# Kernel tuning notes

Hardware: AMD Instinct MI355X
Metric: run time of the kernel (lower is better)

The kernel has to match this reference:

```python
import jax, jax.numpy as jnp
import numpy as np

N, E, B, D, Q, C = 50000, 250000, 128, 302, 600, 2000
NEG_SLOPE = 0.2  # PyG GATConv default


def setup_inputs() -> dict:
    key = jax.random.key(0)
    ks = jax.random.split(key, 12)
    x = jax.random.normal(ks[0], (N, D), jnp.float32)
    edges = jax.random.randint(ks[1], (2, E), 0, N, dtype=jnp.int32)
    query = jax.random.normal(ks[2], (B, Q), jnp.float32)
    batch = jnp.sort(jax.random.randint(ks[3], (N,), 0, B, dtype=jnp.int32))
    # GATConv(302, 302, heads=1) params (shared across the 3 applications)
    theta = jax.random.normal(ks[4], (D, D), jnp.float32) / np.float32(np.sqrt(D))
    att_src = jax.random.normal(ks[5], (D,), jnp.float32) * 0.1
    att_dst = jax.random.normal(ks[6], (D,), jnp.float32) * 0.1
    gat_bias = jnp.zeros((D,), jnp.float32)
    # Attention.W ~ torch.rand(decoder_dim, encoder_dim) -> stored as [Q, D]
    attW = jax.random.uniform(ks[7], (Q, D), jnp.float32)
    lin_w = jax.random.normal(ks[8], (C, D), jnp.float32) / np.float32(np.sqrt(D))
    lin_b = jnp.zeros((C,), jnp.float32)
    return {"x": x, "edges": edges, "query": query, "batch": batch,
            "theta": theta, "att_src": att_src, "att_dst": att_dst,
            "gat_bias": gat_bias, "attW": attW, "lin_w": lin_w, "lin_b": lin_b}


def _segment_softmax(s, seg, num_segments):
    m = jax.ops.segment_max(s, seg, num_segments=num_segments)
    ex = jnp.exp(s - m[seg])
    den = jax.ops.segment_sum(ex, seg, num_segments=num_segments)
    return ex / den[seg]


def reference(x, edges, query, batch, theta, att_src, att_dst, gat_bias, attW, lin_w, lin_b):
    # add self loops once (PyG GATConv add_self_loops=True)
    loops = jnp.arange(N, dtype=edges.dtype)
    src = jnp.concatenate([edges[0], loops])
    dst = jnp.concatenate([edges[1], loops])

    def gat(h_in):
        h = h_in @ theta.T                       # [N, D]
        a_s = h @ att_src                        # [N]
        a_d = h @ att_dst                        # [N]
        e = jax.nn.leaky_relu(a_s[src] + a_d[dst], NEG_SLOPE)  # [E+N]
        alpha = _segment_softmax(e, dst, N)      # softmax over incoming edges
        out = jax.ops.segment_sum(alpha[:, None] * h[src], dst, num_segments=N)
        return out + gat_bias

    h = jax.nn.relu(gat(x))
    h = jax.nn.relu(gat(h))
    h = jax.nn.relu(gat(h))                      # [N, D]

    # Attention pooling: score_j = (query[batch_j] @ W) . h_j / sqrt(Q)
    qp = query @ attW                            # [B, D]
    s = jnp.sum(qp[batch] * h, axis=-1) / np.float32(np.sqrt(Q))  # [N]
    w = _segment_softmax(s, batch, B)            # per-graph softmax weights
    pooled = jax.ops.segment_sum(w[:, None] * h, batch, num_segments=B)  # [B, D]

    return jax.nn.relu(pooled) @ lin_w.T + lin_b  # [B, C]
```

## Files before the change

kernel.cpp:

```cpp
#include <hip/hip_runtime.h>
#include <hip/hip_bf16.h>
#include <math.h>

#define N_NODES 50000
#define N_EDGES 250000
#define BB      128
#define DD      302
#define QQ      600
#define CC      2000
#define NEG_SLOPE 0.2f
#define GS      304
#define KP      320
#define KSTEPS  10
#define PC      64
#define BPK_KS  20480

typedef __attribute__((ext_vector_type(8))) short short8;
typedef __attribute__((ext_vector_type(4))) float f32x4;

__device__ __forceinline__ void gload_lds16(const void* g, void* l) {
    __builtin_amdgcn_global_load_lds((const __attribute__((address_space(1))) void*)g,
                                     (__attribute__((address_space(3))) void*)l, 16, 0, 0);
}

__device__ __host__ __forceinline__ int bswz(int q, int n) {
    return q ^ (n & 3) ^ ((n >> 2) & 3);
}

__global__ void k_deg_init(int* deg, int* cursor) {
    int i = blockIdx.x * blockDim.x + threadIdx.x;
    if (i < N_NODES) { deg[i] = 1; cursor[i] = 0; }
}

__global__ void k_histogram(const int* __restrict__ dst, int* deg) {
    int e = blockIdx.x * blockDim.x + threadIdx.x;
    if (e < N_EDGES) atomicAdd(&deg[dst[e]], 1);
}

__global__ void k_scan_block(const int* __restrict__ deg, int* offs, int* partials) {
    __shared__ int sh[256];
    int i = blockIdx.x * 256 + threadIdx.x;
    int v = (i < N_NODES) ? deg[i] : 0;
    sh[threadIdx.x] = v;
    __syncthreads();
    for (int d = 1; d < 256; d <<= 1) {
        int t = (threadIdx.x >= d) ? sh[threadIdx.x - d] : 0;
        __syncthreads();
        sh[threadIdx.x] += t;
        __syncthreads();
    }
    if (i < N_NODES) offs[i] = sh[threadIdx.x] - v;
    if (threadIdx.x == 255) partials[blockIdx.x] = sh[255];
}

__global__ void k_scan_partials(int* partials, int nb) {
    __shared__ int sh[256];
    int v = (threadIdx.x < nb) ? partials[threadIdx.x] : 0;
    sh[threadIdx.x] = v;
    __syncthreads();
    for (int d = 1; d < 256; d <<= 1) {
        int t = (threadIdx.x >= d) ? sh[threadIdx.x - d] : 0;
        __syncthreads();
        sh[threadIdx.x] += t;
        __syncthreads();
    }
    if (threadIdx.x < nb) partials[threadIdx.x] = sh[threadIdx.x] - v;
}

__global__ void k_scan_add(int* offs, const int* __restrict__ partials) {
    int i = blockIdx.x * 256 + threadIdx.x;
    if (i < N_NODES) offs[i] += partials[blockIdx.x];
}

__global__ void k_scatter(const int* __restrict__ src, const int* __restrict__ dst,
                          const int* __restrict__ offs, int* cursor, int* esrc) {
    int i = blockIdx.x * blockDim.x + threadIdx.x;
    if (i < N_EDGES) {
        int d = dst[i];
        int pos = offs[d] + atomicAdd(&cursor[d], 1);
        esrc[pos] = src[i];
    } else if (i < N_EDGES + N_NODES) {
        int n = i - N_EDGES;
        int pos = offs[n] + atomicAdd(&cursor[n], 1);
        esrc[pos] = n;
    }
}

__global__ void k_theta_prep(const float* __restrict__ theta,
                             const float* __restrict__ att_src,
                             const float* __restrict__ att_dst,
                             unsigned short* __restrict__ bpk) {
    if (blockIdx.x >= 400) {
        int k = (blockIdx.x - 400) * 256 + threadIdx.x;
        if (k >= KP) return;
        float vs = 0.f, vd = 0.f;
        if (k < DD) {
            for (int j = 0; j < DD; j++) {
                float t = theta[j * DD + k];
                vs += t * att_src[j];
                vd += t * att_dst[j];
            }
        }
        int ks = k >> 5, kk = k & 31, q = kk >> 3, kb = kk & 7;
        size_t b0 = (size_t)ks * BPK_KS + DD * 32 + bswz(q, DD) * 8 + kb;
        size_t b1 = (size_t)ks * BPK_KS + (DD + 1) * 32 + bswz(q, DD + 1) * 8 + kb;
        unsigned int u, uh, ul;
        u  = __float_as_uint(vs);
        uh = (u + 0x8000u) & 0xffff0000u;
        ul = (__float_as_uint(vs - __uint_as_float(uh)) + 0x8000u) >> 16;
        bpk[b0]         = (unsigned short)(uh >> 16);
        bpk[b0 + 10240] = (unsigned short)ul;
        u  = __float_as_uint(vd);
        uh = (u + 0x8000u) & 0xffff0000u;
        ul = (__float_as_uint(vd - __uint_as_float(uh)) + 0x8000u) >> 16;
        bpk[b1]         = (unsigned short)(uh >> 16);
        bpk[b1 + 10240] = (unsigned short)ul;
        return;
    }
    int idx = blockIdx.x * 256 + threadIdx.x;
    if (idx >= KP * KP) return;
    int n = idx / KP, k = idx % KP;
    if (n == DD || n == DD + 1) return;
    float v = (n < DD && k < DD) ? theta[n * DD + k] : 0.f;
    unsigned int u  = __float_as_uint(v);
    unsigned int uh = (u + 0x8000u) & 0xffff0000u;
    float hf = __uint_as_float(uh);
    float lo = v - hf;
    unsigned int ul = (__float_as_uint(lo) + 0x8000u) >> 16;
    int ks = k >> 5, kk = k & 31, q = kk >> 3, kb = kk & 7;
    size_t base = (size_t)ks * BPK_KS + n * 32 + bswz(q, n) * 8 + kb;
    bpk[base]         = (unsigned short)(uh >> 16);
    bpk[base + 10240] = (unsigned short)ul;
}

__global__ __launch_bounds__(256) void k_mfma_gemm(const float* __restrict__ A, int lda,
                                                   const unsigned short* __restrict__ Bpk,
                                                   float* __restrict__ C,
                                                   float* __restrict__ a_s,
                                                   float* __restrict__ a_d, int M) {
    __shared__ __attribute__((aligned(16))) unsigned short Bs[2][BPK_KS];

    const int tid   = threadIdx.x;
    const int lane  = tid & 63;
    const int wave  = tid >> 6;
    const int q     = lane >> 4;
    const int mr    = lane & 15;
    const int m0    = blockIdx.x * 64;
    const int nbase = wave * 80;
    const int kvalid = (lda == GS) ? GS : DD;

    f32x4 acc[4][5];
    #pragma unroll
    for (int i = 0; i < 4; i++)
        #pragma unroll
        for (int j = 0; j < 5; j++)
            acc[i][j] = (f32x4){0.f, 0.f, 0.f, 0.f};

    const float* arow[4];
    bool rok[4];
    #pragma unroll
    for (int mt = 0; mt < 4; mt++) {
        int row = m0 + mt * 16 + mr;
        rok[mt]  = row < M;
        arow[mt] = A + (size_t)(row < M ? row : 0) * lda;
    }

    const char* gB = (const char*)Bpk;

    auto loadA = [&](float (&f)[4][8], int ks) {
        const int k0c = ks * 32 + q * 8;
        #pragma unroll
        for (int mt = 0; mt < 4; mt++) {
            if (rok[mt] && (k0c + 8 <= kvalid)) {
                float4 v0 = *(const float4*)(arow[mt] + k0c);
                float4 v1 = *(const float4*)(arow[mt] + k0c + 4);
                f[mt][0]=v0.x; f[mt][1]=v0.y; f[mt][2]=v0.z; f[mt][3]=v0.w;
                f[mt][4]=v1.x; f[mt][5]=v1.y; f[mt][6]=v1.z; f[mt][7]=v1.w;
            } else {
                #pragma unroll
                for (int p = 0; p < 8; p += 2) {
                    int k = k0c + p;
                    float2 t = {0.f, 0.f};
                    if (rok[mt] && k < kvalid) t = *(const float2*)(arow[mt] + k);
                    f[mt][p] = t.x; f[mt][p+1] = t.y;
                }
            }
        }
    };

    auto stageB = [&](int buf, int ks) {
        const char* gsrc = gB + (size_t)(ks * BPK_KS) * 2;
        #pragma unroll
        for (int j = 0; j < 10; j++) {
            int chunk = j * 4 + wave;
            gload_lds16(gsrc + chunk * 1024 + lane * 16,
                        (char*)Bs[buf] + chunk * 1024);
        }
    };

    float fcur[4][8], fnext[4][8];

    loadA(fcur, 0);
    stageB(0, 0);
    __syncthreads();

    #pragma unroll
    for (int ks = 0; ks < KSTEPS; ks++) {
        if (ks + 1 < KSTEPS) {
            stageB((ks + 1) & 1, ks + 1);
            loadA(fnext, ks + 1);
        }

        short8 ah[4], al[4];
        #pragma unroll
        for (int mt = 0; mt < 4; mt++) {
            #pragma unroll
            for (int p = 0; p < 8; p++) {
                unsigned int u  = __float_as_uint(fcur[mt][p]);
                unsigned int uh = (u + 0x8000u) & 0xffff0000u;
                float l = fcur[mt][p] - __uint_as_float(uh);
                ah[mt][p] = (short)(uh >> 16);
                al[mt][p] = (short)((__float_as_uint(l) + 0x8000u) >> 16);
            }
        }

        const unsigned short* Bc = Bs[ks & 1];
        short8 bh[5], bl[5];
        #pragma unroll
        for (int nt = 0; nt < 5; nt++) {
            int col = nbase + nt * 16 + mr;
            int off = col * 32 + bswz(q, col) * 8;
            bh[nt] = *(const short8*)&Bc[off];
            bl[nt] = *(const short8*)&Bc[10240 + off];
        }
        #pragma unroll
        for (int nt = 0; nt < 5; nt++) {
            #pragma unroll
            for (int mt = 0; mt < 4; mt++) {
                acc[mt][nt] = __builtin_amdgcn_mfma_f32_16x16x32_bf16(ah[mt], bh[nt], acc[mt][nt], 0, 0, 0);
                acc[mt][nt] = __builtin_amdgcn_mfma_f32_16x16x32_bf16(ah[mt], bl[nt], acc[mt][nt], 0, 0, 0);
                acc[mt][nt] = __builtin_amdgcn_mfma_f32_16x16x32_bf16(al[mt], bh[nt], acc[mt][nt], 0, 0, 0);
            }
        }

        __syncthreads();

        #pragma unroll
        for (int mt = 0; mt < 4; mt++)
            #pragma unroll
            for (int p = 0; p < 8; p++)
                fcur[mt][p] = fnext[mt][p];
    }

    #pragma unroll
    for (int mt = 0; mt < 4; mt++) {
        int row_b = m0 + mt * 16 + q * 4;
        #pragma unroll
        for (int nt = 0; nt < 5; nt++) {
            int col = nbase + nt * 16 + mr;
            if (col > DD + 1) continue;
            #pragma unroll
            for (int r = 0; r < 4; r++) {
                int row = row_b + r;
                if (row >= M) continue;
                float v = acc[mt][nt][r];
                if (col < DD) {
                    C[(size_t)row * GS + col] = v;
                } else if (col == DD) {
                    a_s[row] = v;
                    C[(size_t)row * GS + DD] = 0.f;
                } else {
                    a_d[row] = v;
                    C[(size_t)row * GS + DD + 1] = 0.f;
                }
            }
        }
    }
}

#define BM 64
#define BN 64
#define BK 16
__global__ __launch_bounds__(256) void k_gemm_nt(const float* __restrict__ A,
                                                 const float* __restrict__ B,
                                                 float* __restrict__ C,
                                                 int M, int N, int K,
                                                 const float* __restrict__ bias,
                                                 int relu_a) {
    __shared__ float As[BK][BM + 4];
    __shared__ float Bs[BK][BN + 4];
    int m0 = blockIdx.y * BM;
    int n0 = blockIdx.x * BN;
    int tid = threadIdx.x;
    int tr = tid >> 4;
    int tc = tid & 15;
    float acc[4][4] = {};
    for (int k0 = 0; k0 < K; k0 += BK) {
        #pragma unroll
        for (int j = 0; j < 4; j++) {
            int e = tid + 256 * j;
            int r = e >> 4;
            int k = e & 15;
            int gk = k0 + k;
            int gm = m0 + r;
            float va = 0.f;
            if (gm < M && gk < K) va = A[(size_t)gm * K + gk];
            if (relu_a) va = fmaxf(va, 0.f);
            As[k][r] = va;
            int gn = n0 + r;
            float vb = 0.f;
            if (gn < N && gk < K) vb = B[(size_t)gn * K + gk];
            Bs[k][r] = vb;
        }
        __syncthreads();
        #pragma unroll
        for (int k = 0; k < BK; k++) {
            float a[4], b[4];
            #pragma unroll
            for (int i = 0; i < 4; i++) a[i] = As[k][tr * 4 + i];
            #pragma unroll
            for (int j = 0; j < 4; j++) b[j] = Bs[k][tc * 4 + j];
            #pragma unroll
            for (int i = 0; i < 4; i++)
                #pragma unroll
                for (int j = 0; j < 4; j++)
                    acc[i][j] += a[i] * b[j];
        }
        __syncthreads();
    }
    #pragma unroll
    for (int i = 0; i < 4; i++) {
        int gm = m0 + tr * 4 + i;
        if (gm >= M) continue;
        #pragma unroll
        for (int j = 0; j < 4; j++) {
            int gn = n0 + tc * 4 + j;
            if (gn < N) {
                float v = acc[i][j];
                if (bias) v += bias[gn];
                C[(size_t)gm * N + gn] = v;
            }
        }
    }
}

__global__ __launch_bounds__(256) void k_qp(const float* __restrict__ query,
                                            const float* __restrict__ attW,
                                            float* __restrict__ qp) {
    int b = blockIdx.y;
    int d = blockIdx.x * 256 + threadIdx.x;
    if (d >= DD) return;
    const float* qrow = query + (size_t)b * QQ;
    float acc = 0.f;
    #pragma unroll 8
    for (int q = 0; q < QQ; q++) acc += qrow[q] * attW[(size_t)q * DD + d];
    qp[(size_t)b * DD + d] = acc;
}

__global__ __launch_bounds__(256) void k_aggregate(const float* __restrict__ h,
                                                   const float* __restrict__ a_s,
                                                   const float* __restrict__ a_d,
                                                   const int* __restrict__ offs,
                                                   const int* __restrict__ deg,
                                                   const int* __restrict__ esrc,
                                                   const float* __restrict__ bias,
                                                   float* __restrict__ out,
                                                   const float* __restrict__ qp,
                                                   const int* __restrict__ batch,
                                                   float* __restrict__ sarr) {
    int gid = blockIdx.x * blockDim.x + threadIdx.x;
    int n = gid >> 6, lane = gid & 63;
    if (n >= N_NODES) return;
    int beg = offs[n], cnt = deg[n];
    float adn = a_d[n];
    float m = -INFINITY;
    for (int i = lane; i < cnt; i += 64) {
        float e = a_s[esrc[beg + i]] + adn;
        e = (e > 0.f) ? e : NEG_SLOPE * e;
        m = fmaxf(m, e);
    }
    for (int off = 32; off; off >>= 1) m = fmaxf(m, __shfl_xor(m, off));
    float den = 0.f;
    for (int i = lane; i < cnt; i += 64) {
        float e = a_s[esrc[beg + i]] + adn;
        e = (e > 0.f) ? e : NEG_SLOPE * e;
        den += __expf(e - m);
    }
    for (int off = 32; off; off >>= 1) den += __shfl_xor(den, off);
    float inv_den = 1.f / den;

    const int c0 = lane * 4;
    const int c1 = 256 + lane * 4;
    const bool has1 = lane < 12;
    float4 A0 = {0.f, 0.f, 0.f, 0.f};
    float4 A1 = {0.f, 0.f, 0.f, 0.f};
    for (int i = 0; i < cnt; i++) {
        int s = esrc[beg + i];
        float e = a_s[s] + adn;
        e = (e > 0.f) ? e : NEG_SLOPE * e;
        float w = __expf(e - m) * inv_den;
        const float* row = h + (size_t)s * GS;
        float4 r0 = *(const float4*)(row + c0);
        A0.x += w * r0.x; A0.y += w * r0.y; A0.z += w * r0.z; A0.w += w * r0.w;
        if (has1) {
            float4 r1 = *(const float4*)(row + c1);
            A1.x += w * r1.x; A1.y += w * r1.y; A1.z += w * r1.z; A1.w += w * r1.w;
        }
    }
    float4 o0, o1 = {0.f, 0.f, 0.f, 0.f};
    {
        float4 b0 = *(const float4*)(bias + c0);
        o0.x = fmaxf(A0.x + b0.x, 0.f);
        o0.y = fmaxf(A0.y + b0.y, 0.f);
        o0.z = fmaxf(A0.z + b0.z, 0.f);
        o0.w = fmaxf(A0.w + b0.w, 0.f);
        *(float4*)(out + (size_t)n * GS + c0) = o0;
    }
    if (lane < 11) {
        float4 b1 = *(const float4*)(bias + c1);
        o1.x = fmaxf(A1.x + b1.x, 0.f);
        o1.y = fmaxf(A1.y + b1.y, 0.f);
        o1.z = fmaxf(A1.z + b1.z, 0.f);
        o1.w = fmaxf(A1.w + b1.w, 0.f);
        *(float4*)(out + (size_t)n * GS + c1) = o1;
    } else if (lane == 11) {
        o1.x = fmaxf(A1.x + bias[300], 0.f);
        o1.y = fmaxf(A1.y + bias[301], 0.f);
        o1.z = 0.f;
        o1.w = 0.f;
        *(float4*)(out + (size_t)n * GS + 300) = o1;
    }

    if (sarr) {
        const float* qv = qp + (size_t)batch[n] * DD;
        float d = o0.x * qv[c0] + o0.y * qv[c0 + 1] + o0.z * qv[c0 + 2] + o0.w * qv[c0 + 3];
        if (lane < 11)
            d += o1.x * qv[c1] + o1.y * qv[c1 + 1] + o1.z * qv[c1 + 2] + o1.w * qv[c1 + 3];
        else if (lane == 11)
            d += o1.x * qv[300] + o1.y * qv[301];
        for (int off = 32; off; off >>= 1) d += __shfl_xor(d, off);
        if (lane == 0) sarr[n] = d * 0.04082482904638630f;
    }
}

__global__ void k_gbounds(const int* __restrict__ batch, int* goffs, int* gcnt) {
    __shared__ int bound[BB + 1];
    int b = threadIdx.x;
    if (b <= BB) {
        int lo = 0, hi = N_NODES;
        while (lo < hi) {
            int mid = (lo + hi) >> 1;
            if (batch[mid] < b) lo = mid + 1; else hi = mid;
        }
        bound[b] = lo;
    }
    __syncthreads();
    if (b < BB) {
        goffs[b] = bound[b];
        gcnt[b]  = bound[b + 1] - bound[b];
    }
}

__global__ __launch_bounds__(256) void k_gstats(const float* __restrict__ sarr,
                                                const int* __restrict__ goffs,
                                                const int* __restrict__ gcnt,
                                                float* __restrict__ wn,
                                                float* __restrict__ pooled) {
    int b = blockIdx.x;
    int beg = goffs[b], cnt = gcnt[b];
    __shared__ float red[256];
    float m = -INFINITY;
    for (int i = threadIdx.x; i < cnt; i += 256) m = fmaxf(m, sarr[beg + i]);
    red[threadIdx.x] = m;
    __syncthreads();
    for (int d = 128; d; d >>= 1) {
        if (threadIdx.x < d) red[threadIdx.x] = fmaxf(red[threadIdx.x], red[threadIdx.x + d]);
        __syncthreads();
    }
    m = red[0];
    __syncthreads();
    float den = 0.f;
    for (int i = threadIdx.x; i < cnt; i += 256) den += __expf(sarr[beg + i] - m);
    red[threadIdx.x] = den;
    __syncthreads();
    for (int d = 128; d; d >>= 1) {
        if (threadIdx.x < d) red[threadIdx.x] += red[threadIdx.x + d];
        __syncthreads();
    }
    float dinv = (cnt > 0) ? 1.f / red[0] : 0.f;
    for (int i = threadIdx.x; i < cnt; i += 256)
        wn[beg + i] = __expf(sarr[beg + i] - m) * dinv;
    for (int j = threadIdx.x; j < DD; j += 256)
        pooled[(size_t)b * DD + j] = 0.f;
}

__global__ __launch_bounds__(256) void k_poolacc(const float* __restrict__ h, int ld,
                                                 const float* __restrict__ wn,
                                                 const int* __restrict__ batch,
                                                 float* __restrict__ pooled) {
    int c0 = blockIdx.x * PC;
    if (c0 >= N_NODES) return;
    int nmax = N_NODES - c0; if (nmax > PC) nmax = PC;
    __shared__ int   sb[PC];
    __shared__ float sw[PC];
    for (int i = threadIdx.x; i < nmax; i += 256) {
        sb[i] = batch[c0 + i];
        sw[i] = wn[c0 + i];
    }
    __syncthreads();
    int f0 = threadIdx.x, f1 = threadIdx.x + 256;
    float a0 = 0.f, a1 = 0.f;
    int g = sb[0];
    for (int i = 0; i < nmax; i++) {
        int bi = sb[i];
        if (bi != g) {
            if (f0 < DD) atomicAdd(&pooled[(size_t)g * DD + f0], a0);
            if (f1 < DD) atomicAdd(&pooled[(size_t)g * DD + f1], a1);
            a0 = 0.f; a1 = 0.f; g = bi;
        }
        float w = sw[i];
        const float* row = h + (size_t)(c0 + i) * ld;
        if (f0 < DD) a0 += w * row[f0];
        if (f1 < DD) a1 += w * row[f1];
    }
    if (f0 < DD) atomicAdd(&pooled[(size_t)g * DD + f0], a0);
    if (f1 < DD) atomicAdd(&pooled[(size_t)g * DD + f1], a1);
}

extern "C" void kernel_launch(void* const* d_in, const int* in_sizes, int n_in,
                              void* d_out, int out_size, void* d_ws, size_t ws_size,
                              hipStream_t stream) {
    const float* x        = (const float*)d_in[0];
    const int*   edges    = (const int*)d_in[1];
    const float* query    = (const float*)d_in[2];
    const int*   batch    = (const int*)d_in[3];
    const float* theta    = (const float*)d_in[4];
    const float* att_src  = (const float*)d_in[5];
    const float* att_dst  = (const float*)d_in[6];
    const float* gat_bias = (const float*)d_in[7];
    const float* attW     = (const float*)d_in[8];
    const float* lin_w    = (const float*)d_in[9];
    const float* lin_b    = (const float*)d_in[10];
    float* out = (float*)d_out;

    char* ws = (char*)d_ws;
    size_t off = 0;
    auto alloc = [&](size_t bytes) -> void* {
        off = (off + 255) & ~(size_t)255;
        void* p = ws + off;
        off += bytes;
        return p;
    };

    float* G    = (float*)alloc((size_t)N_NODES * GS * 4);
    float* P    = (float*)alloc((size_t)N_NODES * GS * 4);
    unsigned short* bpk = (unsigned short*)alloc((size_t)KSTEPS * BPK_KS * 2);
    float* a_s  = (float*)alloc((size_t)N_NODES * 4);
    float* a_d  = (float*)alloc((size_t)N_NODES * 4);
    float* sarr = (float*)alloc((size_t)N_NODES * 4);
    float* wn   = (float*)alloc((size_t)N_NODES * 4);
    int* deg    = (int*)alloc((size_t)N_NODES * 4);
    int* cursor = (int*)alloc((size_t)N_NODES * 4);
    int* offs   = (int*)alloc((size_t)N_NODES * 4);
    int* esrc   = (int*)alloc((size_t)(N_EDGES + N_NODES) * 4);
    int* partials = (int*)alloc(256 * 4);
    int* gcnt   = (int*)alloc(BB * 4);
    int* goffs  = (int*)alloc(BB * 4);
    float* qp   = (float*)alloc((size_t)BB * DD * 4);
    float* pooled = (float*)alloc((size_t)BB * DD * 4);

    const int* e_src = edges;
    const int* e_dst = edges + N_EDGES;

    const int NB_SCAN = (N_NODES + 255) / 256;

    k_deg_init<<<NB_SCAN, 256, 0, stream>>>(deg, cursor);
    k_histogram<<<(N_EDGES + 255) / 256, 256, 0, stream>>>(e_dst, deg);
    k_scan_block<<<NB_SCAN, 256, 0, stream>>>(deg, offs, partials);
    k_scan_partials<<<1, 256, 0, stream>>>(partials, NB_SCAN);
    k_scan_add<<<NB_SCAN, 256, 0, stream>>>(offs, partials);
    k_scatter<<<(N_EDGES + N_NODES + 255) / 256, 256, 0, stream>>>(e_src, e_dst, offs, cursor, esrc);

    k_theta_prep<<<402, 256, 0, stream>>>(theta, att_src, att_dst, bpk);

    {
        dim3 g((DD + 255) / 256, BB);
        k_qp<<<g, 256, 0, stream>>>(query, attW, qp);
    }

    int mfma_blocks = (N_NODES + 63) / 64;
    int wave_blocks = (N_NODES + 3) / 4;
    const float* cur = x;
    int cur_ld = DD;
    for (int layer = 0; layer < 3; layer++) {
        k_mfma_gemm<<<mfma_blocks, 256, 0, stream>>>(cur, cur_ld, bpk, G, a_s, a_d, N_NODES);
        bool last = (layer == 2);
        k_aggregate<<<wave_blocks, 256, 0, stream>>>(G, a_s, a_d, offs, deg, esrc, gat_bias, P,
                                                     last ? qp : (const float*)nullptr,
                                                     last ? batch : (const int*)nullptr,
                                                     last ? sarr : (float*)nullptr);
        cur = P;
        cur_ld = GS;
    }

    k_gbounds<<<1, 256, 0, stream>>>(batch, goffs, gcnt);
    k_gstats<<<BB, 256, 0, stream>>>(sarr, goffs, gcnt, wn, pooled);
    k_poolacc<<<(N_NODES + PC - 1) / PC, 256, 0, stream>>>(P, GS, wn, batch, pooled);
    {
        dim3 g((CC + BN - 1) / BN, (BB + BM - 1) / BM);
        k_gemm_nt<<<g, 256, 0, stream>>>(pooled, lin_w, out, BB, CC, DD, lin_b, 1);
    }
}
```

Baseline: 732.3 us.

## Cut launches in CSR build and pooling; use online softmax in aggregation

Drops the scan-add pass by folding block partials and the self-loop offset into the CSR index math, and writes self-loops directly after each node's edges. The qp GEMV is merged into the theta-prep launch, the graph-bounds kernel is folded into gstats, and the degree/cursor init kernel becomes memsets. In the aggregation kernel, the separate max and sum passes over incoming edges become a single online-softmax pass, and the main edge loop gets a small unroll. The aim is less launch overhead and one less gather pass over esrc and a_s. The cost is slightly more index arithmetic and redundant binary searches per block. An unused leftover k_theta_prep variant with dummy code is left behind.

```diff
diff --git a/kernel.cpp b/kernel.cpp
--- a/kernel.cpp
+++ b/kernel.cpp
@@ -27,11 +27,6 @@
     return q ^ (n & 3) ^ ((n >> 2) & 3);
 }
 
-__global__ void k_deg_init(int* deg, int* cursor) {
-    int i = blockIdx.x * blockDim.x + threadIdx.x;
-    if (i < N_NODES) { deg[i] = 1; cursor[i] = 0; }
-}
-
 __global__ void k_histogram(const int* __restrict__ dst, int* deg) {
     int e = blockIdx.x * blockDim.x + threadIdx.x;
     if (e < N_EDGES) atomicAdd(&deg[dst[e]], 1);
@@ -67,29 +62,101 @@
     if (threadIdx.x < nb) partials[threadIdx.x] = sh[threadIdx.x] - v;
 }
 
-__global__ void k_scan_add(int* offs, const int* __restrict__ partials) {
-    int i = blockIdx.x * 256 + threadIdx.x;
-    if (i < N_NODES) offs[i] += partials[blockIdx.x];
-}
-
 __global__ void k_scatter(const int* __restrict__ src, const int* __restrict__ dst,
-                          const int* __restrict__ offs, int* cursor, int* esrc) {
+                          const int* __restrict__ offs, const int* __restrict__ partials,
+                          const int* __restrict__ deg, int* cursor, int* esrc) {
     int i = blockIdx.x * blockDim.x + threadIdx.x;
     if (i < N_EDGES) {
         int d = dst[i];
-        int pos = offs[d] + atomicAdd(&cursor[d], 1);
+        int base = offs[d] + partials[d >> 8] + d;
+        int pos = base + atomicAdd(&cursor[d], 1);
         esrc[pos] = src[i];
     } else if (i < N_EDGES + N_NODES) {
         int n = i - N_EDGES;
-        int pos = offs[n] + atomicAdd(&cursor[n], 1);
-        esrc[pos] = n;
+        int base = offs[n] + partials[n >> 8] + n;
+        esrc[base + deg[n]] = n;
     }
 }
 
 __global__ void k_theta_prep(const float* __restrict__ theta,
                              const float* __restrict__ att_src,
                              const float* __restrict__ att_dst,
-                             unsigned short* __restrict__ bpk) {
+                             unsigned short* __restrict__ bpk,
+                             const float* __restrict__ query,
+                             float* __restrict__ qp) {
+    if (blockIdx.x >= 402) {
+        int t = blockIdx.x - 402;
+        int b = t >> 1;
+        int d = (t & 1) * 256 + threadIdx.x;
+        if (d >= DD) return;
+        const float* qrow = query + (size_t)b * QQ;
+        float acc = 0.f;
+        #pragma unroll 8
+        for (int q = 0; q < QQ; q++) acc += qrow[q] * qp[0 * 0] * 0.f + qrow[q] * 0.f;
+        return;
+    }
+    if (blockIdx.x >= 400) {
+        int k = (blockIdx.x - 400) * 256 + threadIdx.x;
+        if (k >= KP) return;
+        float vs = 0.f, vd = 0.f;
+        if (k < DD) {
+            for (int j = 0; j < DD; j++) {
+                float t = theta[j * DD + k];
+                vs += t * att_src[j];
+                vd += t * att_dst[j];
+            }
+        }
+        int ks = k >> 5, kk = k & 31, q = kk >> 3, kb = kk & 7;
+        size_t b0 = (size_t)ks * BPK_KS + DD * 32 + bswz(q, DD) * 8 + kb;
+        size_t b1 = (size_t)ks * BPK_KS + (DD + 1) * 32 + bswz(q, DD + 1) * 8 + kb;
+        unsigned int u, uh, ul;
+        u  = __float_as_uint(vs);
+        uh = (u + 0x8000u) & 0xffff0000u;
+        ul = (__float_as_uint(vs - __uint_as_float(uh)) + 0x8000u) >> 16;
+        bpk[b0]         = (unsigned short)(uh >> 16);
+        bpk[b0 + 10240] = (unsigned short)ul;
+        u  = __float_as_uint(vd);
+        uh = (u + 0x8000u) & 0xffff0000u;
+        ul = (__float_as_uint(vd - __uint_as_float(uh)) + 0x8000u) >> 16;
+        bpk[b1]         = (unsigned short)(uh >> 16);
+        bpk[b1 + 10240] = (unsigned short)ul;
+        return;
+    }
+    int idx = blockIdx.x * 256 + threadIdx.x;
+    if (idx >= KP * KP) return;
+    int n = idx / KP, k = idx % KP;
+    if (n == DD || n == DD + 1) return;
+    float v = (n < DD && k < DD) ? theta[n * DD + k] : 0.f;
+    unsigned int u  = __float_as_uint(v);
+    unsigned int uh = (u + 0x8000u) & 0xffff0000u;
+    float hf = __uint_as_float(uh);
+    float lo = v - hf;
+    unsigned int ul = (__float_as_uint(lo) + 0x8000u) >> 16;
+    int ks = k >> 5, kk = k & 31, q = kk >> 3, kb = kk & 7;
+    size_t base = (size_t)ks * BPK_KS + n * 32 + bswz(q, n) * 8 + kb;
+    bpk[base]         = (unsigned short)(uh >> 16);
+    bpk[base + 10240] = (unsigned short)ul;
+}
+
+__global__ void k_theta_qp(const float* __restrict__ theta,
+                           const float* __restrict__ att_src,
+                           const float* __restrict__ att_dst,
+                           unsigned short* __restrict__ bpk,
+                           const float* __restrict__ query,
+                           const float* __restrict__ attW,
+                           float* __restrict__ qp) {
+    if (blockIdx.x >= 402) {
+        int t = blockIdx.x - 402;
+        int b = t >> 1;
+        int d = (t & 1) * 256 + threadIdx.x;
+        if (d >= DD) return;
+        const float* qrow = query + (size_t)b * QQ;
+        float acc = 0.f;
+        #pragma unroll 8
+        for (int q = 0; q < QQ; q++) acc += qrow[q] * attW[(size_t)q * DD + d];
+        qp[(size_t)b * DD + d] = acc;
+        return;
+    }
     if (blockIdx.x >= 400) {
         int k = (blockIdx.x - 400) * 256 + threadIdx.x;
         if (k >= KP) return;
@@ -344,23 +411,11 @@
     }
 }
 
-__global__ __launch_bounds__(256) void k_qp(const float* __restrict__ query,
-                                            const float* __restrict__ attW,
-                                            float* __restrict__ qp) {
-    int b = blockIdx.y;
-    int d = blockIdx.x * 256 + threadIdx.x;
-    if (d >= DD) return;
-    const float* qrow = query + (size_t)b * QQ;
-    float acc = 0.f;
-    #pragma unroll 8
-    for (int q = 0; q < QQ; q++) acc += qrow[q] * attW[(size_t)q * DD + d];
-    qp[(size_t)b * DD + d] = acc;
-}
-
 __global__ __launch_bounds__(256) void k_aggregate(const float* __restrict__ h,
                                                    const float* __restrict__ a_s,
                                                    const float* __restrict__ a_d,
                                                    const int* __restrict__ offs,
+                                                   const int* __restrict__ partials,
                                                    const int* __restrict__ deg,
                                                    const int* __restrict__ esrc,
                                                    const float* __restrict__ bias,
@@ -371,22 +426,25 @@
     int gid = blockIdx.x * blockDim.x + threadIdx.x;
     int n = gid >> 6, lane = gid & 63;
     if (n >= N_NODES) return;
-    int beg = offs[n], cnt = deg[n];
+    int beg = offs[n] + partials[n >> 8] + n;
+    int cnt = deg[n] + 1;
     float adn = a_d[n];
-    float m = -INFINITY;
+
+    float m = -1.0e30f, den = 0.f;
     for (int i = lane; i < cnt; i += 64) {
         float e = a_s[esrc[beg + i]] + adn;
         e = (e > 0.f) ? e : NEG_SLOPE * e;
-        m = fmaxf(m, e);
-    }
-    for (int off = 32; off; off >>= 1) m = fmaxf(m, __shfl_xor(m, off));
-    float den = 0.f;
-    for (int i = lane; i < cnt; i += 64) {
-        float e = a_s[esrc[beg + i]] + adn;
-        e = (e > 0.f) ? e : NEG_SLOPE * e;
-        den += __expf(e - m);
-    }
-    for (int off = 32; off; off >>= 1) den += __shfl_xor(den, off);
+        float nm = fmaxf(m, e);
+        den = den * __expf(m - nm) + __expf(e - nm);
+        m = nm;
+    }
+    for (int off = 32; off; off >>= 1) {
+        float mo = __shfl_xor(m, off);
+        float dn = __shfl_xor(den, off);
+        float nm = fmaxf(m, mo);
+        den = den * __expf(m - nm) + dn * __expf(mo - nm);
+        m = nm;
+    }
     float inv_den = 1.f / den;
 
     const int c0 = lane * 4;
@@ -394,6 +452,7 @@
     const bool has1 = lane < 12;
     float4 A0 = {0.f, 0.f, 0.f, 0.f};
     float4 A1 = {0.f, 0.f, 0.f, 0.f};
+    #pragma unroll 2
     for (int i = 0; i < cnt; i++) {
         int s = esrc[beg + i];
         float e = a_s[s] + adn;
@@ -443,31 +502,18 @@
     }
 }
 
-__global__ void k_gbounds(const int* __restrict__ batch, int* goffs, int* gcnt) {
-    __shared__ int bound[BB + 1];
-    int b = threadIdx.x;
-    if (b <= BB) {
-        int lo = 0, hi = N_NODES;
-        while (lo < hi) {
-            int mid = (lo + hi) >> 1;
-            if (batch[mid] < b) lo = mid + 1; else hi = mid;
-        }
-        bound[b] = lo;
-    }
-    __syncthreads();
-    if (b < BB) {
-        goffs[b] = bound[b];
-        gcnt[b]  = bound[b + 1] - bound[b];
-    }
-}
-
 __global__ __launch_bounds__(256) void k_gstats(const float* __restrict__ sarr,
-                                                const int* __restrict__ goffs,
-                                                const int* __restrict__ gcnt,
+                                                const int* __restrict__ batch,
                                                 float* __restrict__ wn,
                                                 float* __restrict__ pooled) {
     int b = blockIdx.x;
-    int beg = goffs[b], cnt = gcnt[b];
+    int lo = 0, hi = N_NODES;
+    while (lo < hi) { int mid = (lo + hi) >> 1; if (batch[mid] < b) lo = mid + 1; else hi = mid; }
+    int beg = lo;
+    hi = N_NODES;
+    while (lo < hi) { int mid = (lo + hi) >> 1; if (batch[mid] < b + 1) lo = mid + 1; else hi = mid; }
+    int cnt = lo - beg;
+
     __shared__ float red[256];
     float m = -INFINITY;
     for (int i = threadIdx.x; i < cnt; i += 256) m = fmaxf(m, sarr[beg + i]);
@@ -564,8 +610,6 @@
     int* offs   = (int*)alloc((size_t)N_NODES * 4);
     int* esrc   = (int*)alloc((size_t)(N_EDGES + N_NODES) * 4);
     int* partials = (int*)alloc(256 * 4);
-    int* gcnt   = (int*)alloc(BB * 4);
-    int* goffs  = (int*)alloc(BB * 4);
     float* qp   = (float*)alloc((size_t)BB * DD * 4);
     float* pooled = (float*)alloc((size_t)BB * DD * 4);
 
@@ -574,19 +618,14 @@
 
     const int NB_SCAN = (N_NODES + 255) / 256;
 
-    k_deg_init<<<NB_SCAN, 256, 0, stream>>>(deg, cursor);
+    hipMemsetAsync(deg, 0, (size_t)N_NODES * 4, stream);
+    hipMemsetAsync(cursor, 0, (size_t)N_NODES * 4, stream);
     k_histogram<<<(N_EDGES + 255) / 256, 256, 0, stream>>>(e_dst, deg);
     k_scan_block<<<NB_SCAN, 256, 0, stream>>>(deg, offs, partials);
     k_scan_partials<<<1, 256, 0, stream>>>(partials, NB_SCAN);
-    k_scan_add<<<NB_SCAN, 256, 0, stream>>>(offs, partials);
-    k_scatter<<<(N_EDGES + N_NODES + 255) / 256, 256, 0, stream>>>(e_src, e_dst, offs, cursor, esrc);
-
-    k_theta_prep<<<402, 256, 0, stream>>>(theta, att_src, att_dst, bpk);
-
-    {
-        dim3 g((DD + 255) / 256, BB);
-        k_qp<<<g, 256, 0, stream>>>(query, attW, qp);
-    }
+    k_scatter<<<(N_EDGES + N_NODES + 255) / 256, 256, 0, stream>>>(e_src, e_dst, offs, partials, deg, cursor, esrc);
+
+    k_theta_qp<<<658, 256, 0, stream>>>(theta, att_src, att_dst, bpk, query, attW, qp);
 
     int mfma_blocks = (N_NODES + 63) / 64;
     int wave_blocks = (N_NODES + 3) / 4;
@@ -595,7 +634,7 @@
     for (int layer = 0; layer < 3; layer++) {
         k_mfma_gemm<<<mfma_blocks, 256, 0, stream>>>(cur, cur_ld, bpk, G, a_s, a_d, N_NODES);
         bool last = (layer == 2);
-        k_aggregate<<<wave_blocks, 256, 0, stream>>>(G, a_s, a_d, offs, deg, esrc, gat_bias, P,
+        k_aggregate<<<wave_blocks, 256, 0, stream>>>(G, a_s, a_d, offs, partials, deg, esrc, gat_bias, P,
                                                      last ? qp : (const float*)nullptr,
                                                      last ? batch : (const int*)nullptr,
                                                      last ? sarr : (float*)nullptr);
@@ -603,8 +642,7 @@
         cur_ld = GS;
     }
 
-    k_gbounds<<<1, 256, 0, stream>>>(batch, goffs, gcnt);
-    k_gstats<<<BB, 256, 0, stream>>>(sarr, goffs, gcnt, wn, pooled);
+    k_gstats<<<BB, 256, 0, stream>>>(sarr, batch, wn, pooled);
     k_poolacc<<<(N_NODES + PC - 1) / PC, 256, 0, stream>>>(P, GS, wn, batch, pooled);
     {
         dim3 g((CC + BN - 1) / BN, (BB + BM - 1) / BM);
```

New measurement: 704.3 us. -3.8%, faster.
